# Kernel tuning notes

Hardware: AMD Instinct MI355X
Metric: run time of the kernel (lower is better)

The kernel has to match this reference:

```python
import jax, jax.numpy as jnp
import numpy as np

SLOPE = 25.0  # fast-sigmoid surrogate slope (snntorch default)

@jax.custom_vjp
def spike(u):
    # Heaviside spike with fast-sigmoid surrogate gradient
    return (u > 0).astype(u.dtype)

def _spike_fwd(u):
    return spike(u), u

def _spike_bwd(u, g):
    return (g / (1.0 + SLOPE * jnp.abs(u)) ** 2,)

spike.defvjp(_spike_fwd, _spike_bwd)


def setup_inputs() -> dict:
    key = jax.random.key(0)
    B, N_IN, T = 256, 700, 100
    H1, H2, O = 2048, 2048, 20
    ks = jax.random.split(key, 6)

    def lin(k, out_d, in_d):
        s = 1.0 / np.sqrt(in_d)
        kw, kb = jax.random.split(k)
        W = jax.random.uniform(kw, (out_d, in_d), minval=-s, maxval=s, dtype=jnp.float32)
        b = jax.random.uniform(kb, (out_d,), minval=-s, maxval=s, dtype=jnp.float32)
        return W, b

    W1, b1 = lin(ks[0], H1, N_IN)
    W2, b2 = lin(ks[1], H2, H1)
    V, _ = lin(ks[2], H2, H2)  # learned recurrent weight of RecurrentAhpc
    W3, b3 = lin(ks[3], O, H2)
    data = jax.random.normal(ks[4], (B, N_IN, T), dtype=jnp.float32)
    f32 = lambda v: jnp.asarray(v, jnp.float32)
    return dict(
        data=data,
        W1=W1, b1=b1, W2=W2, b2=b2, V=V, W3=W3, b3=b3,
        beta1=f32(0.9), thr1=f32(1.0),
        beta_r=f32(0.9), thr_r=f32(1.0),
        back_beta=f32(0.85), alpha=f32(0.6),
        beta2=f32(0.9), thr2=f32(1.0),
    )


def _forward(data, W1, b1, W2, b2, V, W3, b3,
             beta1, thr1, beta_r, thr_r, back_beta, alpha, beta2, thr2):
    B = data.shape[0]
    H1, H2, O = W1.shape[0], W2.shape[0], W3.shape[0]
    xs = jnp.transpose(data, (2, 0, 1))  # [T, B, N_in]
    z = lambda d: jnp.zeros((B, d), dtype=data.dtype)
    init = (z(H1), z(H2), z(H2), z(H2), z(O))  # mem1, mem_r, ahp, spk_r, mem2

    def step(carry, x_t):
        mem1, mem_r, ahp, spk_r, mem2 = carry
        # layer 1: Linear + Leaky (reset-by-subtract)
        mem1 = beta1 * mem1 + x_t @ W1.T + b1
        s1 = spike(mem1 - thr1)
        mem1 = mem1 - s1 * thr1
        # layer 2: Linear + recurrent AHP leaky neuron
        cur = s1 @ W2.T + b2 + spk_r @ V.T
        mem_r = beta_r * mem_r + cur - ahp
        s_r = spike(mem_r - thr_r)
        mem_r = mem_r - s_r * thr_r
        ahp = back_beta * ahp + alpha * s_r  # after-hyperpolarization current
        # layer 3: Linear + Leaky output
        mem2 = beta2 * mem2 + s_r @ W3.T + b3
        s2 = spike(mem2 - thr2)
        mem2 = mem2 - s2 * thr2
        return (mem1, mem_r, ahp, s_r, mem2), s2

    _, spk_rec = jax.lax.scan(step, init, xs)
    return spk_rec  # [T, B, num_outputs]


def reference(data, W1, b1, W2, b2, V, W3, b3,
              beta1, thr1, beta_r, thr_r, back_beta, alpha, beta2, thr2):
    return _forward(data, W1, b1, W2, b2, V, W3, b3,
                    beta1, thr1, beta_r, thr_r, back_beta, alpha, beta2, thr2)
```

## Files before the change

kernel.cpp:

```cpp
#include <hip/hip_runtime.h>
#include <hip/hip_bf16.h>
#include <cstdint>

#define T_STEPS 100
#define BATCH 256
#define NIN 700
#define H1 2048
#define H2 2048
#define NOUT 20
#define VKS 8
#define TCHUNK 10

typedef __attribute__((ext_vector_type(8))) short bf16x8;
typedef __attribute__((ext_vector_type(4))) float f32x4;
typedef unsigned long long ull;

__device__ __forceinline__ void async16(void* lds, const void* g) {
    __builtin_amdgcn_global_load_lds(
        (const __attribute__((address_space(1))) unsigned int*)g,
        (__attribute__((address_space(3))) unsigned int*)lds, 16, 0, 0);
}

__device__ __forceinline__ unsigned short f2bf(float x) {
    __hip_bfloat16 h = __float2bfloat16(x);
    return *(unsigned short*)&h;
}
__device__ __forceinline__ float bf2f(unsigned short u) {
    __hip_bfloat16 h = *(__hip_bfloat16*)&u;
    return __bfloat162float(h);
}

__global__ __launch_bounds__(256) void split_kernel(
    const float* __restrict__ W2, const float* __restrict__ V,
    unsigned short* __restrict__ Bsplit)
{
    const size_t D = (size_t)2048 * 4096;
    size_t i = (size_t)blockIdx.x * 256 + threadIdx.x;
    int j = (int)(i >> 12), k = (int)(i & 4095);
    float w = (k < 2048) ? W2[(size_t)j * 2048 + k] : V[(size_t)j * 2048 + (k - 2048)];
    unsigned short h = f2bf(w);
    float r1 = w - bf2f(h);
    unsigned short m = f2bf(r1);
    float r2 = r1 - bf2f(m);
    unsigned short l = f2bf(r2);
    Bsplit[i] = h;
    Bsplit[D + i] = m;
    Bsplit[2 * D + i] = l;
}

__global__ __launch_bounds__(256) void w1split_kernel(
    const float* __restrict__ W1, unsigned short* __restrict__ W1f)
{
    const size_t P = (size_t)88 * 2048 * 8;
    int id = blockIdx.x * 256 + threadIdx.x;
    int g = id >> 11, j = id & 2047;
    unsigned short h8[8], m8[8], l8[8];
    #pragma unroll
    for (int e = 0; e < 8; ++e) {
        int k = g * 8 + e;
        float v = (k < NIN) ? W1[(size_t)j * NIN + k] : 0.f;
        unsigned short h = f2bf(v); float r1 = v - bf2f(h);
        unsigned short m = f2bf(r1); float r2 = r1 - bf2f(m);
        h8[e] = h; m8[e] = m; l8[e] = f2bf(r2);
    }
    size_t base = (((size_t)g * 2048) + j) * 8;
    *(uint4*)(W1f + base)         = *(uint4*)h8;
    *(uint4*)(W1f + P + base)     = *(uint4*)m8;
    *(uint4*)(W1f + 2 * P + base) = *(uint4*)l8;
}

__global__ __launch_bounds__(256) void l1m_kernel(
    const float* __restrict__ data, const unsigned short* __restrict__ W1f,
    const float* __restrict__ b1,
    const float* __restrict__ p_beta1, const float* __restrict__ p_thr1,
    ull* __restrict__ s1bits)
{
    __shared__ __align__(16) char smem[33280];
    unsigned short* Af = (unsigned short*)smem;
    const int tid = threadIdx.x, lane = tid & 63, w = tid >> 6;
    const int n16 = lane & 15, q = lane >> 4;
    const int jt = blockIdx.x & 7, b = blockIdx.x >> 3;
    const int j0w = jt * 256 + w * 64;
    const float* xb = data + (size_t)b * (NIN * T_STEPS);
    const size_t P = (size_t)88 * 2048 * 8;

    f32x4 acc[7][4] = {};
    for (int c = 0; c < 22; ++c) {
        const int kbase = c * 32;
        for (int it = tid; it < 448; it += 256) {
            int g = it / 112, t = it - g * 112;
            unsigned short h8[8], m8[8], l8[8];
            #pragma unroll
            for (int e = 0; e < 8; ++e) {
                int k = kbase + g * 8 + e;
                float v = (t < T_STEPS && k < NIN) ? xb[(size_t)k * T_STEPS + t] : 0.f;
                unsigned short h = f2bf(v); float r1 = v - bf2f(h);
                unsigned short m = f2bf(r1); float r2 = r1 - bf2f(m);
                h8[e] = h; m8[e] = m; l8[e] = f2bf(r2);
            }
            unsigned short* dst = Af + g * 896 + t * 8;
            *(uint4*)(dst)        = *(uint4*)h8;
            *(uint4*)(dst + 3584) = *(uint4*)m8;
            *(uint4*)(dst + 7168) = *(uint4*)l8;
        }
        __syncthreads();
        bf16x8 bh[4], bm[4], bl[4];
        const size_t gq = (size_t)(c * 4 + q);
        #pragma unroll
        for (int n = 0; n < 4; ++n) {
            size_t off = (gq * 2048 + (size_t)(j0w + n * 16 + n16)) * 8;
            bh[n] = *(const bf16x8*)(W1f + off);
            bm[n] = *(const bf16x8*)(W1f + P + off);
            bl[n] = *(const bf16x8*)(W1f + 2 * P + off);
        }
        #pragma unroll
        for (int m = 0; m < 7; ++m) {
            const unsigned short* ap = Af + q * 896 + (m * 16 + n16) * 8;
            bf16x8 ah = *(const bf16x8*)(ap);
            bf16x8 am = *(const bf16x8*)(ap + 3584);
            bf16x8 al = *(const bf16x8*)(ap + 7168);
            #pragma unroll
            for (int n = 0; n < 4; ++n) {
                acc[m][n] = __builtin_amdgcn_mfma_f32_16x16x32_bf16(ah, bh[n], acc[m][n], 0, 0, 0);
                acc[m][n] = __builtin_amdgcn_mfma_f32_16x16x32_bf16(ah, bm[n], acc[m][n], 0, 0, 0);
                acc[m][n] = __builtin_amdgcn_mfma_f32_16x16x32_bf16(am, bh[n], acc[m][n], 0, 0, 0);
                acc[m][n] = __builtin_amdgcn_mfma_f32_16x16x32_bf16(ah, bl[n], acc[m][n], 0, 0, 0);
                acc[m][n] = __builtin_amdgcn_mfma_f32_16x16x32_bf16(al, bh[n], acc[m][n], 0, 0, 0);
                acc[m][n] = __builtin_amdgcn_mfma_f32_16x16x32_bf16(am, bm[n], acc[m][n], 0, 0, 0);
            }
        }
        __syncthreads();
    }
    float* Cw = (float*)smem + w * (32 * 65);
    const float beta1 = *p_beta1, thr1 = *p_thr1;
    const float b1j = b1[j0w + lane];
    float mem = 0.f;
    for (int s = 0; s < 4; ++s) {
        #pragma unroll
        for (int mm = 0; mm < 2; ++mm) {
            int m = s * 2 + mm;
            if (m < 7) {
                #pragma unroll
                for (int n = 0; n < 4; ++n)
                    #pragma unroll
                    for (int r = 0; r < 4; ++r)
                        Cw[(mm * 16 + q * 4 + r) * 65 + n * 16 + n16] = acc[m][n][r];
            }
        }
        int tcnt = (s < 3) ? 32 : 4;
        for (int tt = 0; tt < tcnt; ++tt) {
            float v = Cw[tt * 65 + lane];
            mem = fmaf(beta1, mem, v) + b1j;
            bool pred = (mem - thr1) > 0.f;
            ull mask = __ballot(pred);
            if (pred) mem -= thr1;
            if (lane == 0) {
                int tg = s * 32 + tt;
                s1bits[((size_t)tg * BATCH + b) * 32 + jt * 4 + w] = mask;
            }
        }
    }
}

__global__ __launch_bounds__(256) void expand_kernel(
    const ull* __restrict__ bits_t0,
    unsigned short* __restrict__ plane)
{
    const int row = blockIdx.x;
    const int tid = threadIdx.x;
    ull word = bits_t0[(size_t)row * 32 + (tid >> 3)];
    unsigned int byte = (unsigned int)(word >> ((tid & 7) * 8)) & 0xFFu;
    unsigned short o8[8];
    #pragma unroll
    for (int e = 0; e < 8; ++e)
        o8[e] = (byte >> e) & 1u ? (unsigned short)0x3F80 : (unsigned short)0;
    *(uint4*)(plane + (size_t)row * 2048 + tid * 8) = *(uint4*)o8;
}

__global__ __launch_bounds__(256, 2) void xw2_kernel(
    const unsigned short* __restrict__ S1c,
    const unsigned short* __restrict__ Bsplit,
    float* __restrict__ X2c)
{
    __shared__ __align__(16) unsigned short Alds[256 * 64];
    __shared__ __align__(16) unsigned short Blds[3 * 64 * 64];
    const int bid = blockIdx.x;
    const int x = bid & 7;
    const int i = bid >> 3;
    const int ntl = i / TCHUNK;
    const int mt = i - ntl * TCHUNK;
    const int n0 = (x * 4 + ntl) << 6;
    const int tid = threadIdx.x, lane = tid & 63, w = tid >> 6;
    const unsigned short* Abase = S1c + ((size_t)mt << 8) * 2048;
    f32x4 acc[4][4] = {};
    for (int c = 0; c < 32; ++c) {
        const int kin = c << 6;
        #pragma unroll
        for (int ii = 0; ii < 8; ++ii) {
            int gi = (ii << 8) + tid;
            int row = gi >> 3, g8 = gi & 7;
            async16(Alds + ((size_t)gi << 3),
                    Abase + (size_t)row * 2048 + kin + ((g8 ^ (row & 7)) << 3));
        }
        #pragma unroll
        for (int term = 0; term < 3; ++term) {
            const unsigned short* Bg = Bsplit + ((size_t)term << 23);
            #pragma unroll
            for (int ii = 0; ii < 2; ++ii) {
                int d = (w << 7) + (ii << 6) + lane;
                int row = d >> 3, g8 = d & 7;
                async16(Blds + (((term << 9) + (w << 7) + (ii << 6)) << 3),
                        Bg + (size_t)(n0 + row) * 4096 + kin + ((g8 ^ (row & 7)) << 3));
            }
        }
        __syncthreads();
        #pragma unroll
        for (int kk = 0; kk < 2; ++kk) {
            const int q = lane >> 4, k16 = (kk << 2) + q;
            bf16x8 af[4];
            #pragma unroll
            for (int ii = 0; ii < 4; ++ii) {
                int ra = (w << 6) + (ii << 4) + (lane & 15);
                af[ii] = *(const bf16x8*)(Alds + (((ra << 3) + (k16 ^ (ra & 7))) << 3));
            }
            #pragma unroll
            for (int term = 0; term < 3; ++term) {
                bf16x8 bfr[4];
                #pragma unroll
                for (int j = 0; j < 4; ++j) {
                    int rb = (j << 4) + (lane & 15);
                    bfr[j] = *(const bf16x8*)(Blds +
                              (((term << 9) + (rb << 3) + (k16 ^ (rb & 7))) << 3));
                }
                #pragma unroll
                for (int ii = 0; ii < 4; ++ii)
                    #pragma unroll
                    for (int j = 0; j < 4; ++j)
                        acc[ii][j] = __builtin_amdgcn_mfma_f32_16x16x32_bf16(
                            af[ii], bfr[j], acc[ii][j], 0, 0, 0);
            }
        }
        __syncthreads();
    }
    float* Xp = X2c + ((size_t)mt << 8) * 2048;
    #pragma unroll
    for (int ii = 0; ii < 4; ++ii) {
        int rg = (w << 6) + (ii << 4) + ((lane >> 4) << 2);
        #pragma unroll
        for (int j = 0; j < 4; ++j) {
            int cg = n0 + (j << 4) + (lane & 15);
            #pragma unroll
            for (int r = 0; r < 4; ++r)
                Xp[(size_t)(rg + r) * 2048 + cg] = acc[ii][j][r];
        }
    }
}

__global__ __launch_bounds__(256, 2) void vgemm_kernel(
    const unsigned short* __restrict__ spk,
    const unsigned short* __restrict__ Bsplit,
    float* __restrict__ Cpart)
{
    __shared__ __align__(16) unsigned short Alds[256 * 64];
    __shared__ __align__(16) unsigned short Blds[3 * 64 * 64];
    const int bid = blockIdx.x;
    const int nt = bid & 31, ks = bid >> 5;
    const int n0 = nt << 6;
    const int tid = threadIdx.x, lane = tid & 63, w = tid >> 6;
    f32x4 acc[4][4] = {};
    for (int c = 0; c < 4; ++c) {
        const int kin = (ks << 8) + (c << 6);
        #pragma unroll
        for (int ii = 0; ii < 8; ++ii) {
            int gi = (ii << 8) + tid;
            int row = gi >> 3, g8 = gi & 7;
            async16(Alds + ((size_t)gi << 3),
                    spk + (size_t)row * 2048 + kin + ((g8 ^ (row & 7)) << 3));
        }
        #pragma unroll
        for (int term = 0; term < 3; ++term) {
            const unsigned short* Bg = Bsplit + ((size_t)term << 23);
            #pragma unroll
            for (int ii = 0; ii < 2; ++ii) {
                int d = (w << 7) + (ii << 6) + lane;
                int row = d >> 3, g8 = d & 7;
                async16(Blds + (((term << 9) + (w << 7) + (ii << 6)) << 3),
                        Bg + (size_t)(n0 + row) * 4096 + 2048 + kin + ((g8 ^ (row & 7)) << 3));
            }
        }
        __syncthreads();
        #pragma unroll
        for (int kk = 0; kk < 2; ++kk) {
            const int q = lane >> 4, k16 = (kk << 2) + q;
            bf16x8 af[4];
            #pragma unroll
            for (int ii = 0; ii < 4; ++ii) {
                int ra = (w << 6) + (ii << 4) + (lane & 15);
                af[ii] = *(const bf16x8*)(Alds + (((ra << 3) + (k16 ^ (ra & 7))) << 3));
            }
            #pragma unroll
            for (int term = 0; term < 3; ++term) {
                bf16x8 bfr[4];
                #pragma unroll
                for (int j = 0; j < 4; ++j) {
                    int rb = (j << 4) + (lane & 15);
                    bfr[j] = *(const bf16x8*)(Blds +
                              (((term << 9) + (rb << 3) + (k16 ^ (rb & 7))) << 3));
                }
                #pragma unroll
                for (int ii = 0; ii < 4; ++ii)
                    #pragma unroll
                    for (int j = 0; j < 4; ++j)
                        acc[ii][j] = __builtin_amdgcn_mfma_f32_16x16x32_bf16(
                            af[ii], bfr[j], acc[ii][j], 0, 0, 0);
            }
        }
        __syncthreads();
    }
    float* Cp = Cpart + ((size_t)ks << 19);
    #pragma unroll
    for (int ii = 0; ii < 4; ++ii) {
        int rg = (w << 6) + (ii << 4) + ((lane >> 4) << 2);
        #pragma unroll
        for (int j = 0; j < 4; ++j) {
            int cg = n0 + (j << 4) + (lane & 15);
            #pragma unroll
            for (int r = 0; r < 4; ++r)
                Cp[(size_t)(rg + r) * 2048 + cg] = acc[ii][j][r];
        }
    }
}

__global__ __launch_bounds__(256) void l2fin_kernel(
    const float* __restrict__ Cpart, const float* __restrict__ X2t,
    const float* __restrict__ b2,
    float* __restrict__ mem_r, float* __restrict__ ahp,
    unsigned short* __restrict__ spk_out,
    const float* __restrict__ W3, const float* __restrict__ b3,
    float* __restrict__ mem2, float* __restrict__ out_t,
    const float* __restrict__ p_beta_r, const float* __restrict__ p_thr_r,
    const float* __restrict__ p_back_beta, const float* __restrict__ p_alpha,
    const float* __restrict__ p_beta2, const float* __restrict__ p_thr2)
{
    __shared__ float sLDS[2048];
    __shared__ float red[4][NOUT];
    const int b = blockIdx.x, t = threadIdx.x;
    const int lane = t & 63, wv = t >> 6;
    const float beta_r = *p_beta_r, thr_r = *p_thr_r;
    const float bb = *p_back_beta, al = *p_alpha;
    #pragma unroll
    for (int u = 0; u < 8; ++u) {
        int j = t + (u << 8);
        size_t cidx = (size_t)b * 2048 + j;
        float x = 0.f;
        #pragma unroll
        for (int p = 0; p < VKS; ++p) x += Cpart[((size_t)p << 19) + cidx];
        float cur = x + X2t[cidx] + b2[j];
        float m = fmaf(beta_r, mem_r[cidx], cur) - ahp[cidx];
        bool pred = (m - thr_r) > 0.f;
        float s = pred ? 1.f : 0.f;
        if (pred) m -= thr_r;
        mem_r[cidx] = m;
        ahp[cidx] = fmaf(bb, ahp[cidx], al * s);
        sLDS[j] = s;
        spk_out[cidx] = pred ? (unsigned short)0x3F80 : (unsigned short)0;
    }
    __syncthreads();
    float s8[8];
    #pragma unroll
    for (int i = 0; i < 8; ++i) s8[i] = sLDS[t * 8 + i];
    float po[NOUT];
    #pragma unroll
    for (int o = 0; o < NOUT; ++o) {
        const float4* wp = (const float4*)(W3 + (size_t)o * 2048 + t * 8);
        float4 wa = wp[0], wb2 = wp[1];
        float v = s8[0]*wa.x + s8[1]*wa.y + s8[2]*wa.z + s8[3]*wa.w
                + s8[4]*wb2.x + s8[5]*wb2.y + s8[6]*wb2.z + s8[7]*wb2.w;
        #pragma unroll
        for (int msk = 32; msk > 0; msk >>= 1)
            v += __shfl_xor(v, msk, 64);
        po[o] = v;
    }
    if (lane == 0) {
        #pragma unroll
        for (int o = 0; o < NOUT; ++o) red[wv][o] = po[o];
    }
    __syncthreads();
    if (t < NOUT) {
        const float beta2 = *p_beta2, thr2 = *p_thr2;
        float cur = red[0][t] + red[1][t] + red[2][t] + red[3][t] + b3[t];
        float m = fmaf(beta2, mem2[b * NOUT + t], cur);
        bool pred = (m - thr2) > 0.f;
        float s2 = pred ? 1.f : 0.f;
        if (pred) m -= thr2;
        mem2[b * NOUT + t] = m;
        out_t[b * NOUT + t] = s2;
    }
}

extern "C" void kernel_launch(void* const* d_in, const int* in_sizes, int n_in,
                              void* d_out, int out_size, void* d_ws, size_t ws_size,
                              hipStream_t stream)
{
    const float* data   = (const float*)d_in[0];
    const float* W1     = (const float*)d_in[1];
    const float* b1     = (const float*)d_in[2];
    const float* W2     = (const float*)d_in[3];
    const float* b2     = (const float*)d_in[4];
    const float* V      = (const float*)d_in[5];
    const float* W3     = (const float*)d_in[6];
    const float* b3     = (const float*)d_in[7];
    const float* beta1  = (const float*)d_in[8];
    const float* thr1   = (const float*)d_in[9];
    const float* beta_r = (const float*)d_in[10];
    const float* thr_r  = (const float*)d_in[11];
    const float* back_beta = (const float*)d_in[12];
    const float* alpha  = (const float*)d_in[13];
    const float* beta2  = (const float*)d_in[14];
    const float* thr2   = (const float*)d_in[15];
    float* out = (float*)d_out;
    (void)in_sizes; (void)n_in; (void)out_size; (void)ws_size;

    char* p = (char*)d_ws;
    auto carve = [&](size_t bytes) {
        char* r = p; p += (bytes + 255) & ~(size_t)255; return r;
    };
    ull* s1bits = (ull*)carve((size_t)T_STEPS*BATCH*32*8);
    unsigned short* spk0 = (unsigned short*)carve((size_t)BATCH*H2*2);
    unsigned short* spk1 = (unsigned short*)carve((size_t)BATCH*H2*2);
    float* mem_r = (float*)carve((size_t)BATCH*H2*4);
    float* ahp   = (float*)carve((size_t)BATCH*H2*4);
    float* mem2  = (float*)carve((size_t)BATCH*NOUT*4);
    unsigned short* Bsplit = (unsigned short*)carve((size_t)3*2048*4096*2);
    char* uni = carve((size_t)VKS*BATCH*H2*4);
    unsigned short* S1c = (unsigned short*)uni;
    float* Cpart = (float*)uni;
    float* X2c = (float*)carve((size_t)TCHUNK*BATCH*H2*4);
    unsigned short* W1f = (unsigned short*)carve((size_t)3*88*2048*8*2);

    hipMemsetAsync(spk0, 0, (size_t)BATCH*H2*2, stream);
    hipMemsetAsync(mem_r, 0, (size_t)BATCH*H2*4, stream);
    hipMemsetAsync(ahp,  0, (size_t)BATCH*H2*4, stream);
    hipMemsetAsync(mem2, 0, (size_t)BATCH*NOUT*4, stream);

    split_kernel<<<(2048*4096)/256, 256, 0, stream>>>(W2, V, Bsplit);
    w1split_kernel<<<704, 256, 0, stream>>>(W1, W1f);
    l1m_kernel<<<2048, 256, 0, stream>>>(data, W1f, b1, beta1, thr1, s1bits);

    unsigned short* spk[2] = {spk0, spk1};
    for (int ck = 0; ck < T_STEPS / TCHUNK; ++ck) {
        const int t0 = ck * TCHUNK;
        expand_kernel<<<TCHUNK*BATCH, 256, 0, stream>>>(
            s1bits + (size_t)t0*BATCH*32, S1c);
        xw2_kernel<<<8*4*TCHUNK, 256, 0, stream>>>(S1c, Bsplit, X2c);
        for (int tt = 0; tt < TCHUNK; ++tt) {
            const int t = t0 + tt;
            vgemm_kernel<<<256, 256, 0, stream>>>(spk[t & 1], Bsplit, Cpart);
            l2fin_kernel<<<256, 256, 0, stream>>>(Cpart,
                                                  X2c + (size_t)tt*BATCH*H2, b2,
                                                  mem_r, ahp, spk[(t + 1) & 1],
                                                  W3, b3, mem2,
                                                  out + (size_t)t*BATCH*NOUT,
                                                  beta_r, thr_r, back_beta, alpha,
                                                  beta2, thr2);
        }
    }
}
```

Baseline: 3.610 ms.

## Fuse layer-2 finalize into recurrent GEMM via last-block atomics; defer W3 readout

The separate per-step l2fin kernel is removed. Each vstep block bumps an atomic counter per output-column tile after writing its split-K partial, and the last of the 8 K-split blocks for that tile reduces the partials and updates mem_r, ahp and the spikes. Recurrent spikes are also packed into bitmasks, and a single w3out kernel after the time loop runs the output-layer projection and LIF over all 100 steps. This drops one launch per timestep and takes the serial W3 work off the critical path. In exchange, the finalize runs on only 32 blocks and the design relies on threadfence/atomic ordering being correct.

```diff
diff --git a/kernel.cpp b/kernel.cpp
--- a/kernel.cpp
+++ b/kernel.cpp
@@ -256,13 +256,21 @@
     }
 }
 
-__global__ __launch_bounds__(256, 2) void vgemm_kernel(
+__global__ __launch_bounds__(256, 2) void vstep_kernel(
     const unsigned short* __restrict__ spk,
     const unsigned short* __restrict__ Bsplit,
-    float* __restrict__ Cpart)
+    float* __restrict__ Cpart,
+    const float* __restrict__ X2t, const float* __restrict__ b2,
+    float* __restrict__ mem_r, float* __restrict__ ahp,
+    unsigned short* __restrict__ spk_out,
+    ull* __restrict__ srbits_t,
+    int* __restrict__ done, int expected,
+    const float* __restrict__ p_beta_r, const float* __restrict__ p_thr_r,
+    const float* __restrict__ p_back_beta, const float* __restrict__ p_alpha)
 {
     __shared__ __align__(16) unsigned short Alds[256 * 64];
     __shared__ __align__(16) unsigned short Blds[3 * 64 * 64];
+    __shared__ int lastFlag;
     const int bid = blockIdx.x;
     const int nt = bid & 31, ks = bid >> 5;
     const int n0 = nt << 6;
@@ -329,72 +337,92 @@
                 Cp[(size_t)(rg + r) * 2048 + cg] = acc[ii][j][r];
         }
     }
-}
-
-__global__ __launch_bounds__(256) void l2fin_kernel(
-    const float* __restrict__ Cpart, const float* __restrict__ X2t,
-    const float* __restrict__ b2,
-    float* __restrict__ mem_r, float* __restrict__ ahp,
-    unsigned short* __restrict__ spk_out,
-    const float* __restrict__ W3, const float* __restrict__ b3,
-    float* __restrict__ mem2, float* __restrict__ out_t,
-    const float* __restrict__ p_beta_r, const float* __restrict__ p_thr_r,
-    const float* __restrict__ p_back_beta, const float* __restrict__ p_alpha,
-    const float* __restrict__ p_beta2, const float* __restrict__ p_thr2)
-{
-    __shared__ float sLDS[2048];
-    __shared__ float red[4][NOUT];
-    const int b = blockIdx.x, t = threadIdx.x;
-    const int lane = t & 63, wv = t >> 6;
+    __syncthreads();
+    if (tid == 0) {
+        __threadfence();
+        int old = atomicAdd(&done[nt], 1);
+        lastFlag = (old == expected);
+    }
+    __syncthreads();
+    if (!lastFlag) return;
+    __threadfence();
     const float beta_r = *p_beta_r, thr_r = *p_thr_r;
     const float bb = *p_back_beta, al = *p_alpha;
-    #pragma unroll
-    for (int u = 0; u < 8; ++u) {
-        int j = t + (u << 8);
-        size_t cidx = (size_t)b * 2048 + j;
+    const int jj = n0 + lane;
+    const float b2j = b2[jj];
+    for (int u = 0; u < 64; ++u) {
+        int b = w + (u << 2);
+        size_t cidx = (size_t)b * 2048 + jj;
         float x = 0.f;
         #pragma unroll
         for (int p = 0; p < VKS; ++p) x += Cpart[((size_t)p << 19) + cidx];
-        float cur = x + X2t[cidx] + b2[j];
+        float cur = x + X2t[cidx] + b2j;
         float m = fmaf(beta_r, mem_r[cidx], cur) - ahp[cidx];
         bool pred = (m - thr_r) > 0.f;
+        ull mask = __ballot(pred);
         float s = pred ? 1.f : 0.f;
         if (pred) m -= thr_r;
         mem_r[cidx] = m;
         ahp[cidx] = fmaf(bb, ahp[cidx], al * s);
-        sLDS[j] = s;
         spk_out[cidx] = pred ? (unsigned short)0x3F80 : (unsigned short)0;
-    }
+        if (lane == 0) srbits_t[((size_t)b << 5) + nt] = mask;
+    }
+}
+
+__global__ __launch_bounds__(256) void w3out_kernel(
+    const ull* __restrict__ srbits, const float* __restrict__ W3,
+    const float* __restrict__ b3, float* __restrict__ out,
+    const float* __restrict__ p_beta2, const float* __restrict__ p_thr2)
+{
+    __shared__ ull bitsLDS[T_STEPS * 32];
+    __shared__ float red[4][10];
+    const int b = blockIdx.x, tid = threadIdx.x, lane = tid & 63, wv = tid >> 6;
+    for (int i = tid; i < T_STEPS * 32; i += 256)
+        bitsLDS[i] = srbits[((size_t)(i >> 5) * BATCH + b) * 32 + (i & 31)];
     __syncthreads();
-    float s8[8];
-    #pragma unroll
-    for (int i = 0; i < 8; ++i) s8[i] = sLDS[t * 8 + i];
-    float po[NOUT];
-    #pragma unroll
-    for (int o = 0; o < NOUT; ++o) {
-        const float4* wp = (const float4*)(W3 + (size_t)o * 2048 + t * 8);
-        float4 wa = wp[0], wb2 = wp[1];
-        float v = s8[0]*wa.x + s8[1]*wa.y + s8[2]*wa.z + s8[3]*wa.w
-                + s8[4]*wb2.x + s8[5]*wb2.y + s8[6]*wb2.z + s8[7]*wb2.w;
-        #pragma unroll
-        for (int msk = 32; msk > 0; msk >>= 1)
-            v += __shfl_xor(v, msk, 64);
-        po[o] = v;
-    }
-    if (lane == 0) {
-        #pragma unroll
-        for (int o = 0; o < NOUT; ++o) red[wv][o] = po[o];
-    }
-    __syncthreads();
-    if (t < NOUT) {
-        const float beta2 = *p_beta2, thr2 = *p_thr2;
-        float cur = red[0][t] + red[1][t] + red[2][t] + red[3][t] + b3[t];
-        float m = fmaf(beta2, mem2[b * NOUT + t], cur);
-        bool pred = (m - thr2) > 0.f;
-        float s2 = pred ? 1.f : 0.f;
-        if (pred) m -= thr2;
-        mem2[b * NOUT + t] = m;
-        out_t[b * NOUT + t] = s2;
+    const float beta2 = *p_beta2, thr2 = *p_thr2;
+    for (int pass = 0; pass < 2; ++pass) {
+        float w8[10][8];
+        #pragma unroll
+        for (int o = 0; o < 10; ++o) {
+            const float4* wp = (const float4*)(W3 + (size_t)(pass * 10 + o) * 2048 + tid * 8);
+            float4 a = wp[0], c = wp[1];
+            w8[o][0] = a.x; w8[o][1] = a.y; w8[o][2] = a.z; w8[o][3] = a.w;
+            w8[o][4] = c.x; w8[o][5] = c.y; w8[o][6] = c.z; w8[o][7] = c.w;
+        }
+        float m2 = 0.f;
+        for (int t = 0; t < T_STEPS; ++t) {
+            ull word = bitsLDS[(t << 5) + (tid >> 3)];
+            unsigned int byte = (unsigned int)(word >> ((tid & 7) * 8)) & 0xFFu;
+            float po[10];
+            #pragma unroll
+            for (int o = 0; o < 10; ++o) {
+                float v = 0.f;
+                #pragma unroll
+                for (int e = 0; e < 8; ++e)
+                    v += ((byte >> e) & 1u) ? w8[o][e] : 0.f;
+                #pragma unroll
+                for (int msk = 32; msk > 0; msk >>= 1)
+                    v += __shfl_xor(v, msk, 64);
+                po[o] = v;
+            }
+            if (lane == 0) {
+                #pragma unroll
+                for (int o = 0; o < 10; ++o) red[wv][o] = po[o];
+            }
+            __syncthreads();
+            if (tid < 10) {
+                float cur = red[0][tid] + red[1][tid] + red[2][tid] + red[3][tid]
+                          + b3[pass * 10 + tid];
+                float m = fmaf(beta2, m2, cur);
+                bool pred = (m - thr2) > 0.f;
+                float s2 = pred ? 1.f : 0.f;
+                if (pred) m -= thr2;
+                m2 = m;
+                out[((size_t)t * BATCH + b) * NOUT + pass * 10 + tid] = s2;
+            }
+            __syncthreads();
+        }
     }
 }
 
@@ -426,11 +454,12 @@
         char* r = p; p += (bytes + 255) & ~(size_t)255; return r;
     };
     ull* s1bits = (ull*)carve((size_t)T_STEPS*BATCH*32*8);
+    ull* srbits = (ull*)carve((size_t)T_STEPS*BATCH*32*8);
     unsigned short* spk0 = (unsigned short*)carve((size_t)BATCH*H2*2);
     unsigned short* spk1 = (unsigned short*)carve((size_t)BATCH*H2*2);
     float* mem_r = (float*)carve((size_t)BATCH*H2*4);
     float* ahp   = (float*)carve((size_t)BATCH*H2*4);
-    float* mem2  = (float*)carve((size_t)BATCH*NOUT*4);
+    int* done    = (int*)carve(32 * sizeof(int));
     unsigned short* Bsplit = (unsigned short*)carve((size_t)3*2048*4096*2);
     char* uni = carve((size_t)VKS*BATCH*H2*4);
     unsigned short* S1c = (unsigned short*)uni;
@@ -441,7 +470,7 @@
     hipMemsetAsync(spk0, 0, (size_t)BATCH*H2*2, stream);
     hipMemsetAsync(mem_r, 0, (size_t)BATCH*H2*4, stream);
     hipMemsetAsync(ahp,  0, (size_t)BATCH*H2*4, stream);
-    hipMemsetAsync(mem2, 0, (size_t)BATCH*NOUT*4, stream);
+    hipMemsetAsync(done, 0, 32 * sizeof(int), stream);
 
     split_kernel<<<(2048*4096)/256, 256, 0, stream>>>(W2, V, Bsplit);
     w1split_kernel<<<704, 256, 0, stream>>>(W1, W1f);
@@ -455,14 +484,11 @@
         xw2_kernel<<<8*4*TCHUNK, 256, 0, stream>>>(S1c, Bsplit, X2c);
         for (int tt = 0; tt < TCHUNK; ++tt) {
             const int t = t0 + tt;
-            vgemm_kernel<<<256, 256, 0, stream>>>(spk[t & 1], Bsplit, Cpart);
-            l2fin_kernel<<<256, 256, 0, stream>>>(Cpart,
-                                                  X2c + (size_t)tt*BATCH*H2, b2,
-                                                  mem_r, ahp, spk[(t + 1) & 1],
-                                                  W3, b3, mem2,
-                                                  out + (size_t)t*BATCH*NOUT,
-                                                  beta_r, thr_r, back_beta, alpha,
-                                                  beta2, thr2);
-        }
-    }
-}
+            vstep_kernel<<<256, 256, 0, stream>>>(
+                spk[t & 1], Bsplit, Cpart, X2c + (size_t)tt*BATCH*H2, b2,
+                mem_r, ahp, spk[(t + 1) & 1], srbits + (size_t)t*BATCH*32,
+                done, 8*t + 7, beta_r, thr_r, back_beta, alpha);
+        }
+    }
+    w3out_kernel<<<256, 256, 0, stream>>>(srbits, W3, b3, out, beta2, thr2);
+}
```

After: 7.648 ms. +111.9%, slower.
